# Kernel tuning notes

Measured on AMD Instinct MI355X. Metric: run time of the kernel, lower is better.

Reference implementation:

```python
import jax, jax.numpy as jnp
import numpy as np

B, S, HQ, HKV, DH = 1, 2048, 32, 8, 128
DE = HQ * DH  # DEmbed = 4096
G = HQ // HKV  # GQA group size = 4


def apply_rope(x, cs):
    # x: [B, S, H, DH]; cs: [2, S, 1, DH//2] (broadcast over B via leading dims)
    d = x.shape[-1] // 2
    x1, x2 = x[..., :d], x[..., d:]
    y1 = x1 * cs[0] + x2 * cs[1]
    y2 = -x1 * cs[1] + x2 * cs[0]
    return jnp.concatenate([y1, y2], axis=-1)


def setup_inputs() -> dict:
    key = jax.random.key(0)
    ks = jax.random.split(key, 5)
    x = jax.random.normal(ks[0], (B, S, DE), dtype=jnp.float32)
    # Precomputed rotary tables, shaped [2, S, 1, DH//2] so they broadcast over [B,S,H,DH//2]
    half = DH // 2
    inv_freq = 1.0 / (10000.0 ** (np.arange(half, dtype=np.float64) / half))
    ang = np.arange(S, dtype=np.float64)[:, None] * inv_freq[None, :]
    cos_sin_RoPE = jnp.asarray(
        np.stack([np.cos(ang), np.sin(ang)])[:, :, None, :], dtype=jnp.float32
    )
    sc = DE ** -0.5
    wq = jax.random.normal(ks[1], (DE, HQ * DH), dtype=jnp.float32) * sc
    wk = jax.random.normal(ks[2], (DE, HKV * DH), dtype=jnp.float32) * sc
    wv = jax.random.normal(ks[3], (DE, HKV * DH), dtype=jnp.float32) * sc
    wo = jax.random.normal(ks[4], (DE, DE), dtype=jnp.float32) * sc
    return {"x": x, "cos_sin_RoPE": cos_sin_RoPE, "wq": wq, "wk": wk, "wv": wv, "wo": wo}


def reference(x, cos_sin_RoPE, wq, wk, wv, wo):
    b, s, _ = x.shape
    q = (x @ wq).reshape(b, s, HQ, DH)
    k = (x @ wk).reshape(b, s, HKV, DH)
    v = (x @ wv).reshape(b, s, HKV, DH)
    q = apply_rope(q, cos_sin_RoPE)
    k = apply_rope(k, cos_sin_RoPE)
    # GQA causal SDPA: group query heads per kv head
    q = q.transpose(0, 2, 1, 3).reshape(b, HKV, G, s, DH)  # [b,kv,g,s,d]
    k = k.transpose(0, 2, 1, 3)  # [b,kv,s,d]
    v = v.transpose(0, 2, 1, 3)  # [b,kv,s,d]
    scale = DH ** -0.5
    scores = jnp.einsum('bkgsd,bktd->bkgst', q, k) * scale  # [b,kv,g,s,s]
    mask = jnp.tril(jnp.ones((s, s), dtype=bool))
    scores = jnp.where(mask, scores, jnp.finfo(scores.dtype).min)
    p = jax.nn.softmax(scores, axis=-1)
    o = jnp.einsum('bkgst,bktd->bkgsd', p, v)  # [b,kv,g,s,d]
    o = o.transpose(0, 3, 1, 2, 4).reshape(b, s, HQ * DH)
    return o @ wo
```

## Files before the change

### kernel.cpp

```cpp
#include <hip/hip_runtime.h>
#include <hip/hip_bf16.h>
#include <cstdint>
#include <cstddef>

typedef __bf16 bf16x8 __attribute__((ext_vector_type(8)));
typedef float floatx4 __attribute__((ext_vector_type(4)));

#define MFMA(a, b, c) __builtin_amdgcn_mfma_f32_16x16x32_bf16((a), (b), (c), 0, 0, 0)

__device__ __forceinline__ unsigned short f2bf(float f) {
  unsigned u = __builtin_bit_cast(unsigned, f);
  u += 0x7fffu + ((u >> 16) & 1u);
  return (unsigned short)(u >> 16);
}
__device__ __forceinline__ float bf2f(unsigned short h) {
  unsigned u = ((unsigned)h) << 16;
  return __builtin_bit_cast(float, u);
}
__device__ __forceinline__ float fast_exp2(float x) {
#if __has_builtin(__builtin_amdgcn_exp2f)
  return __builtin_amdgcn_exp2f(x);
#else
  return exp2f(x);
#endif
}

__device__ __forceinline__ void gl2lds16(const unsigned short* g, unsigned short* l) {
  __builtin_amdgcn_global_load_lds(
      (const __attribute__((address_space(1))) unsigned int*)g,
      (__attribute__((address_space(3))) unsigned int*)l, 16, 0, 0);
}

__global__ void convert_f32_bf16(const float* __restrict__ src,
                                 unsigned short* __restrict__ dst, int n4) {
  int i = blockIdx.x * 256 + threadIdx.x;
  if (i >= n4) return;
  float4 f = ((const float4*)src)[i];
  ushort4 o;
  o.x = f2bf(f.x); o.y = f2bf(f.y); o.z = f2bf(f.z); o.w = f2bf(f.w);
  ((ushort4*)dst)[i] = o;
}

__global__ void transpose_f32_bf16(const float* __restrict__ src,
                                   unsigned short* __restrict__ dst, int K, int N) {
  __shared__ float tile[64 * 65];
  int tn = blockIdx.x * 64, tk = blockIdx.y * 64;
  int r = threadIdx.x >> 4;
  int c4 = (threadIdx.x & 15) * 4;
#pragma unroll
  for (int i = 0; i < 4; i++) {
    float4 f = *(const float4*)&src[(size_t)(tk + r + 16 * i) * N + tn + c4];
    float* tr = &tile[(r + 16 * i) * 65 + c4];
    tr[0] = f.x; tr[1] = f.y; tr[2] = f.z; tr[3] = f.w;
  }
  __syncthreads();
#pragma unroll
  for (int i = 0; i < 4; i++) {
    ushort4 o;
    o.x = f2bf(tile[(c4 + 0) * 65 + r + 16 * i]);
    o.y = f2bf(tile[(c4 + 1) * 65 + r + 16 * i]);
    o.z = f2bf(tile[(c4 + 2) * 65 + r + 16 * i]);
    o.w = f2bf(tile[(c4 + 3) * 65 + r + 16 * i]);
    *(ushort4*)&dst[(size_t)(tn + r + 16 * i) * K + tk + c4] = o;
  }
}

template <bool F32OUT>
__global__ __launch_bounds__(256) void gemm_bt(const unsigned short* __restrict__ A,
                        const unsigned short* __restrict__ Bt,
                        void* __restrict__ C, int M, int N, int K) {
  __shared__ alignas(16) unsigned short Alds[128 * 64];
  __shared__ alignas(16) unsigned short Blds[128 * 64];
  const int tid = threadIdx.x;
  const int w = tid >> 6, L = tid & 63;
  const int lr = L & 15, lg = L >> 4;
  const int bm = blockIdx.y * 128, bn = blockIdx.x * 128;
  const int wm = (w >> 1) * 64, wn = (w & 1) * 64;
  floatx4 acc[4][4] = {};

  const int srow = L >> 3;
  const int pcg = L & 7;
  const int scg = (pcg ^ srow) * 8;

  const unsigned short* Ag = &A[(size_t)(bm + w * 32 + srow) * K + scg];
  const unsigned short* Bg = &Bt[(size_t)(bn + w * 32 + srow) * K + scg];
  unsigned short* Al = &Alds[(w * 32 + srow) * 64 + pcg * 8];
  unsigned short* Bl = &Blds[(w * 32 + srow) * 64 + pcg * 8];

  for (int k0 = 0; k0 < K; k0 += 64) {
#pragma unroll
    for (int i = 0; i < 4; i++) {
      gl2lds16(Ag + (size_t)(i * 8) * K, Al + i * 8 * 64);
      gl2lds16(Bg + (size_t)(i * 8) * K, Bl + i * 8 * 64);
    }
    Ag += 64; Bg += 64;
    __syncthreads();

#pragma unroll
    for (int kk = 0; kk < 2; kk++) {
      const int ofs = ((kk * 4 + lg) ^ (lr & 7)) * 8;
      bf16x8 af[4], bfr[4];
#pragma unroll
      for (int i = 0; i < 4; i++) {
        af[i]  = *(const bf16x8*)&Alds[(wm + i * 16 + lr) * 64 + ofs];
        bfr[i] = *(const bf16x8*)&Blds[(wn + i * 16 + lr) * 64 + ofs];
      }
#pragma unroll
      for (int mi = 0; mi < 4; mi++)
#pragma unroll
        for (int ni = 0; ni < 4; ni++)
          acc[mi][ni] = MFMA(af[mi], bfr[ni], acc[mi][ni]);
    }
    __syncthreads();
  }

#pragma unroll
  for (int mi = 0; mi < 4; mi++) {
#pragma unroll
    for (int ni = 0; ni < 4; ni++) {
#pragma unroll
      for (int r = 0; r < 4; r++) {
        size_t row = bm + wm + mi * 16 + lg * 4 + r;
        size_t col = bn + wn + ni * 16 + lr;
        float v = acc[mi][ni][r];
        if constexpr (F32OUT) ((float*)C)[row * N + col] = v;
        else ((unsigned short*)C)[row * N + col] = f2bf(v);
      }
    }
  }
}

__global__ void rope_kernel(unsigned short* __restrict__ X, const float* __restrict__ cs,
                            int H, int rowStride, int colOff, float scale) {
  int idx = blockIdx.x * 256 + threadIdx.x;
  int d = idx & 63;
  int h = (idx >> 6) % H;
  int s = idx / (64 * H);
  size_t base = (size_t)s * rowStride + colOff + (size_t)h * 128;
  float x1 = bf2f(X[base + d]), x2 = bf2f(X[base + d + 64]);
  float c = cs[s * 64 + d];
  float sn = cs[2048 * 64 + s * 64 + d];
  float y1 = (x1 * c + x2 * sn) * scale;
  float y2 = (x2 * c - x1 * sn) * scale;
  X[base + d] = f2bf(y1);
  X[base + d + 64] = f2bf(y2);
}

__global__ void v_transpose(const unsigned short* __restrict__ QKV,
                            unsigned short* __restrict__ Vt) {
  __shared__ unsigned short tile[32][33];
  int h = blockIdx.z;
  int s0 = blockIdx.x * 32, d0 = blockIdx.y * 32;
  int c = threadIdx.x & 31, r0 = threadIdx.x >> 5;
#pragma unroll
  for (int i = 0; i < 32; i += 8)
    tile[r0 + i][c] = QKV[(size_t)(s0 + r0 + i) * 6144 + 5120 + h * 128 + d0 + c];
  __syncthreads();
#pragma unroll
  for (int i = 0; i < 32; i += 8)
    Vt[(size_t)(h * 128 + d0 + r0 + i) * 2048 + s0 + c] = tile[c][r0 + i];
}

__global__ __launch_bounds__(256) void flash_kernel(
    const unsigned short* __restrict__ QKV,
    const unsigned short* __restrict__ Vt,
    unsigned short* __restrict__ O) {
  constexpr int PSTR = 72;
  __shared__ alignas(16) unsigned short Klds[64 * 128];
  __shared__ alignas(16) unsigned short Vlds[128 * 64];
  __shared__ alignas(16) unsigned short Plds[4 * 32 * PSTR];
  const int tid = threadIdx.x, w = tid >> 6, L = tid & 63;
  const int lr = L & 15, lg = L >> 4;
  const int bid = blockIdx.x;
  const int hk = bid & 7;
  const int hp = (bid >> 3) & 1;
  const int qb = 31 - (bid >> 4);
  const int hq = hk * 4 + hp * 2 + (w & 1);
  const int qr0 = qb * 64 + (w >> 1) * 32;
  const unsigned short* Kg = QKV + 4096;

  const int k_row = tid >> 4, k_lcg = tid & 15;
  const unsigned short* KgT = &Kg[(size_t)k_row * 6144 + hk * 128 + ((k_lcg ^ (k_row & 15)) * 8)];
  unsigned short* KlT = &Klds[k_row * 128 + k_lcg * 8];
  const int v_row = tid >> 3, v_lcg = tid & 7;
  const unsigned short* VgT = &Vt[(size_t)(hk * 128 + v_row) * 2048 + ((v_lcg ^ (v_row & 7)) * 8)];
  unsigned short* VlT = &Vlds[v_row * 64 + v_lcg * 8];

  bf16x8 qf[2][4];
#pragma unroll
  for (int mi = 0; mi < 2; mi++)
#pragma unroll
    for (int c = 0; c < 4; c++)
      qf[mi][c] = *(const bf16x8*)&QKV[(size_t)(qr0 + mi * 16 + lr) * 6144 + hq * 128 + c * 32 + lg * 8];

  floatx4 oacc[2][8] = {};
  float l_lane[2][4] = {};
  unsigned short* pw = &Plds[w * 32 * PSTR];

  for (int t = 0; t <= qb; t++) {
    const int kv0 = t * 64;
    __syncthreads();
#pragma unroll
    for (int i = 0; i < 4; i++) {
      gl2lds16(KgT + (size_t)(kv0 + i * 16) * 6144, KlT + i * 16 * 128);
      gl2lds16(VgT + kv0 + (size_t)(i * 32) * 2048, VlT + i * 32 * 64);
    }
    __syncthreads();

#pragma unroll
    for (int nt = 0; nt < 4; nt++) {
      bf16x8 kf[4];
#pragma unroll
      for (int c = 0; c < 4; c++)
        kf[c] = *(const bf16x8*)&Klds[(nt * 16 + lr) * 128 + (((c * 4 + lg) ^ lr) * 8)];
      floatx4 sc[2];
#pragma unroll
      for (int mi = 0; mi < 2; mi++) {
        floatx4 a = {};
#pragma unroll
        for (int c = 0; c < 4; c++) a = MFMA(qf[mi][c], kf[c], a);
        sc[mi] = a;
      }
      if (t == qb) {
#pragma unroll
        for (int mi = 0; mi < 2; mi++)
#pragma unroll
          for (int r = 0; r < 4; r++)
            if (kv0 + nt * 16 + lr > qr0 + mi * 16 + lg * 4 + r) sc[mi][r] = -3e38f;
      }
#pragma unroll
      for (int mi = 0; mi < 2; mi++)
#pragma unroll
        for (int r = 0; r < 4; r++) {
          float p = fast_exp2(sc[mi][r]);
          l_lane[mi][r] += p;
          pw[(mi * 16 + lg * 4 + r) * PSTR + nt * 16 + lr] = f2bf(p);
        }
    }

    bf16x8 pf[2][2];
#pragma unroll
    for (int mi = 0; mi < 2; mi++)
#pragma unroll
      for (int c = 0; c < 2; c++)
        pf[mi][c] = *(const bf16x8*)&pw[(mi * 16 + lr) * PSTR + c * 32 + lg * 8];

#pragma unroll
    for (int n = 0; n < 8; n++) {
#pragma unroll
      for (int c = 0; c < 2; c++) {
        bf16x8 vf = *(const bf16x8*)&Vlds[(n * 16 + lr) * 64 + (((c * 4 + lg) ^ (lr & 7)) * 8)];
#pragma unroll
        for (int mi = 0; mi < 2; mi++) oacc[mi][n] = MFMA(pf[mi][c], vf, oacc[mi][n]);
      }
    }
  }

  float linv[2][4];
#pragma unroll
  for (int mi = 0; mi < 2; mi++)
#pragma unroll
    for (int r = 0; r < 4; r++) {
      float l = l_lane[mi][r];
      l += __shfl_xor(l, 1);
      l += __shfl_xor(l, 2);
      l += __shfl_xor(l, 4);
      l += __shfl_xor(l, 8);
      linv[mi][r] = 1.0f / l;
    }

#pragma unroll
  for (int mi = 0; mi < 2; mi++)
#pragma unroll
    for (int n = 0; n < 8; n++)
#pragma unroll
      for (int r = 0; r < 4; r++) {
        size_t row = qr0 + mi * 16 + lg * 4 + r;
        size_t col = (size_t)hq * 128 + n * 16 + lr;
        O[row * 4096 + col] = f2bf(oacc[mi][n][r] * linv[mi][r]);
      }
}

extern "C" void kernel_launch(void* const* d_in, const int* in_sizes, int n_in,
                              void* d_out, int out_size, void* d_ws, size_t ws_size,
                              hipStream_t stream) {
  const float* x  = (const float*)d_in[0];
  const float* cs = (const float*)d_in[1];
  const float* wq = (const float*)d_in[2];
  const float* wk = (const float*)d_in[3];
  const float* wv = (const float*)d_in[4];
  const float* wo = (const float*)d_in[5];
  float* out = (float*)d_out;

  char* ws = (char*)d_ws;
  unsigned short* xb   = (unsigned short*)(ws);
  unsigned short* wqt  = (unsigned short*)(ws + 16777216);
  unsigned short* wkt  = (unsigned short*)(ws + 50331648);
  unsigned short* wvt  = (unsigned short*)(ws + 58720256);
  unsigned short* wot  = (unsigned short*)(ws + 67108864);
  unsigned short* QKVb = (unsigned short*)(ws + 100663296);
  unsigned short* Vtb  = (unsigned short*)(ws + 125829120);
  unsigned short* Ob   = xb;

  convert_f32_bf16<<<8192, 256, 0, stream>>>(x, xb, 2097152);
  transpose_f32_bf16<<<dim3(64, 64), 256, 0, stream>>>(wq, wqt, 4096, 4096);
  transpose_f32_bf16<<<dim3(16, 64), 256, 0, stream>>>(wk, wkt, 4096, 1024);
  transpose_f32_bf16<<<dim3(16, 64), 256, 0, stream>>>(wv, wvt, 4096, 1024);
  transpose_f32_bf16<<<dim3(64, 64), 256, 0, stream>>>(wo, wot, 4096, 4096);

  gemm_bt<false><<<dim3(48, 16), 256, 0, stream>>>(xb, wqt, QKVb, 2048, 6144, 4096);

  rope_kernel<<<16384, 256, 0, stream>>>(QKVb, cs, 32, 6144, 0, 0.12751743f);
  rope_kernel<<<4096, 256, 0, stream>>>(QKVb, cs, 8, 6144, 4096, 1.0f);

  v_transpose<<<dim3(64, 4, 8), 256, 0, stream>>>(QKVb, Vtb);

  flash_kernel<<<512, 256, 0, stream>>>(QKVb, Vtb, Ob);

  gemm_bt<true><<<dim3(32, 16), 256, 0, stream>>>(Ob, wot, out, 2048, 4096, 4096);
}
```

Before: 500.0 us.

## Compute transposed scores so P feeds PV MFMA from registers, drop P LDS

The QK^T MFMA operands are swapped so each lane holds a column of the score tile. The exponentiated probabilities can then be packed straight into bf16x8 B-operands for the PV MFMA, with no round trip through a per-wave LDS P buffer. V fragments are gathered as two 4-element LDS reads to match the new k-permutation. The row-sum reduction and output stores are adjusted to the transposed layout, with vectorized ushort4 output writes. This removes LDS writes and reads of P and shrinks LDS use, at the cost of more, narrower V LDS reads.

```diff
diff --git a/kernel.cpp b/kernel.cpp
--- a/kernel.cpp
+++ b/kernel.cpp
@@ -5,6 +5,8 @@
 
 typedef __bf16 bf16x8 __attribute__((ext_vector_type(8)));
 typedef float floatx4 __attribute__((ext_vector_type(4)));
+typedef unsigned short ushort4v __attribute__((ext_vector_type(4)));
+typedef unsigned short ushort8v __attribute__((ext_vector_type(8)));
 
 #define MFMA(a, b, c) __builtin_amdgcn_mfma_f32_16x16x32_bf16((a), (b), (c), 0, 0, 0)
 
@@ -165,10 +167,8 @@
     const unsigned short* __restrict__ QKV,
     const unsigned short* __restrict__ Vt,
     unsigned short* __restrict__ O) {
-  constexpr int PSTR = 72;
   __shared__ alignas(16) unsigned short Klds[64 * 128];
   __shared__ alignas(16) unsigned short Vlds[128 * 64];
-  __shared__ alignas(16) unsigned short Plds[4 * 32 * PSTR];
   const int tid = threadIdx.x, w = tid >> 6, L = tid & 63;
   const int lr = L & 15, lg = L >> 4;
   const int bid = blockIdx.x;
@@ -190,12 +190,11 @@
 #pragma unroll
   for (int mi = 0; mi < 2; mi++)
 #pragma unroll
-    for (int c = 0; c < 4; c++)
-      qf[mi][c] = *(const bf16x8*)&QKV[(size_t)(qr0 + mi * 16 + lr) * 6144 + hq * 128 + c * 32 + lg * 8];
+    for (int cd = 0; cd < 4; cd++)
+      qf[mi][cd] = *(const bf16x8*)&QKV[(size_t)(qr0 + mi * 16 + lr) * 6144 + hq * 128 + cd * 32 + lg * 8];
 
   floatx4 oacc[2][8] = {};
-  float l_lane[2][4] = {};
-  unsigned short* pw = &Plds[w * 32 * PSTR];
+  float l_lane[2] = {0.f, 0.f};
 
   for (int t = 0; t <= qb; t++) {
     const int kv0 = t * 64;
@@ -208,77 +207,80 @@
     __syncthreads();
 
 #pragma unroll
-    for (int nt = 0; nt < 4; nt++) {
-      bf16x8 kf[4];
-#pragma unroll
-      for (int c = 0; c < 4; c++)
-        kf[c] = *(const bf16x8*)&Klds[(nt * 16 + lr) * 128 + (((c * 4 + lg) ^ lr) * 8)];
-      floatx4 sc[2];
+    for (int c = 0; c < 2; c++) {
+      floatx4 sc[2][2];
+#pragma unroll
+      for (int ntl = 0; ntl < 2; ntl++) {
+        const int nt = c * 2 + ntl;
+        bf16x8 kf[4];
+#pragma unroll
+        for (int cd = 0; cd < 4; cd++)
+          kf[cd] = *(const bf16x8*)&Klds[(nt * 16 + lr) * 128 + (((cd * 4 + lg) ^ lr) * 8)];
+#pragma unroll
+        for (int mi = 0; mi < 2; mi++) {
+          floatx4 a = {};
+#pragma unroll
+          for (int cd = 0; cd < 4; cd++) a = MFMA(kf[cd], qf[mi][cd], a);
+          sc[ntl][mi] = a;
+        }
+      }
+      if (t == qb) {
+#pragma unroll
+        for (int ntl = 0; ntl < 2; ntl++)
+#pragma unroll
+          for (int mi = 0; mi < 2; mi++)
+#pragma unroll
+            for (int r = 0; r < 4; r++)
+              if (kv0 + (c * 2 + ntl) * 16 + lg * 4 + r > qr0 + mi * 16 + lr)
+                sc[ntl][mi][r] = -3e38f;
+      }
+      bf16x8 pb[2];
 #pragma unroll
       for (int mi = 0; mi < 2; mi++) {
-        floatx4 a = {};
-#pragma unroll
-        for (int c = 0; c < 4; c++) a = MFMA(qf[mi][c], kf[c], a);
-        sc[mi] = a;
-      }
-      if (t == qb) {
-#pragma unroll
-        for (int mi = 0; mi < 2; mi++)
-#pragma unroll
-          for (int r = 0; r < 4; r++)
-            if (kv0 + nt * 16 + lr > qr0 + mi * 16 + lg * 4 + r) sc[mi][r] = -3e38f;
-      }
-#pragma unroll
-      for (int mi = 0; mi < 2; mi++)
-#pragma unroll
-        for (int r = 0; r < 4; r++) {
-          float p = fast_exp2(sc[mi][r]);
-          l_lane[mi][r] += p;
-          pw[(mi * 16 + lg * 4 + r) * PSTR + nt * 16 + lr] = f2bf(p);
-        }
-    }
-
-    bf16x8 pf[2][2];
-#pragma unroll
-    for (int mi = 0; mi < 2; mi++)
-#pragma unroll
-      for (int c = 0; c < 2; c++)
-        pf[mi][c] = *(const bf16x8*)&pw[(mi * 16 + lr) * PSTR + c * 32 + lg * 8];
-
+        ushort8v pu;
+#pragma unroll
+        for (int ntl = 0; ntl < 2; ntl++)
+#pragma unroll
+          for (int r = 0; r < 4; r++) {
+            float p = fast_exp2(sc[ntl][mi][r]);
+            l_lane[mi] += p;
+            pu[ntl * 4 + r] = f2bf(p);
+          }
+        pb[mi] = __builtin_bit_cast(bf16x8, pu);
+      }
+#pragma unroll
+      for (int n = 0; n < 8; n++) {
+        const int row = (n * 16 + lr) * 64;
+        ushort4v vlo = *(const ushort4v*)&Vlds[row + (((c * 4 + (lg >> 1)) ^ (lr & 7)) * 8) + (lg & 1) * 4];
+        ushort4v vhi = *(const ushort4v*)&Vlds[row + (((c * 4 + 2 + (lg >> 1)) ^ (lr & 7)) * 8) + (lg & 1) * 4];
+        ushort8v v8 = __builtin_shufflevector(vlo, vhi, 0, 1, 2, 3, 4, 5, 6, 7);
+        bf16x8 vf = __builtin_bit_cast(bf16x8, v8);
+#pragma unroll
+        for (int mi = 0; mi < 2; mi++) oacc[mi][n] = MFMA(vf, pb[mi], oacc[mi][n]);
+      }
+    }
+  }
+
+  float linv[2];
+#pragma unroll
+  for (int mi = 0; mi < 2; mi++) {
+    float l = l_lane[mi];
+    l += __shfl_xor(l, 16);
+    l += __shfl_xor(l, 32);
+    linv[mi] = 1.0f / l;
+  }
+
+#pragma unroll
+  for (int mi = 0; mi < 2; mi++)
 #pragma unroll
     for (int n = 0; n < 8; n++) {
-#pragma unroll
-      for (int c = 0; c < 2; c++) {
-        bf16x8 vf = *(const bf16x8*)&Vlds[(n * 16 + lr) * 64 + (((c * 4 + lg) ^ (lr & 7)) * 8)];
-#pragma unroll
-        for (int mi = 0; mi < 2; mi++) oacc[mi][n] = MFMA(pf[mi][c], vf, oacc[mi][n]);
-      }
-    }
-  }
-
-  float linv[2][4];
-#pragma unroll
-  for (int mi = 0; mi < 2; mi++)
-#pragma unroll
-    for (int r = 0; r < 4; r++) {
-      float l = l_lane[mi][r];
-      l += __shfl_xor(l, 1);
-      l += __shfl_xor(l, 2);
-      l += __shfl_xor(l, 4);
-      l += __shfl_xor(l, 8);
-      linv[mi][r] = 1.0f / l;
-    }
-
-#pragma unroll
-  for (int mi = 0; mi < 2; mi++)
-#pragma unroll
-    for (int n = 0; n < 8; n++)
-#pragma unroll
-      for (int r = 0; r < 4; r++) {
-        size_t row = qr0 + mi * 16 + lg * 4 + r;
-        size_t col = (size_t)hq * 128 + n * 16 + lr;
-        O[row * 4096 + col] = f2bf(oacc[mi][n][r] * linv[mi][r]);
-      }
+      ushort4 o;
+      o.x = f2bf(oacc[mi][n][0] * linv[mi]);
+      o.y = f2bf(oacc[mi][n][1] * linv[mi]);
+      o.z = f2bf(oacc[mi][n][2] * linv[mi]);
+      o.w = f2bf(oacc[mi][n][3] * linv[mi]);
+      *(ushort4*)&O[(size_t)(qr0 + mi * 16 + lr) * 4096 + hq * 128 + n * 16 + lg * 4] = o;
+    }
 }
 
 extern "C" void kernel_launch(void* const* d_in, const int* in_sizes, int n_in,
```

Result: slower. 516.7 us (+3.3%).
